# Optimization experiments

Hardware: AMD Instinct MI355X
Metric: run time of the kernel (lower is better)

The kernel has to match this reference:

```python
import jax, jax.numpy as jnp
import numpy as np

HEADS = 16
EMBED = 1024
HEAD_DIM = EMBED // HEADS

def _split_heads(x):
    b, n, _ = x.shape
    return x.reshape(b, n, HEADS, HEAD_DIM).transpose(0, 2, 1, 3)  # b h n d

def _merge_heads(x):
    b, h, n, d = x.shape
    return x.transpose(0, 2, 1, 3).reshape(b, n, h * d)

def _attn(q_in, kv_in, Wq, bq, Wk, bk, Wv, bv, Wo, bo):
    q = _split_heads(q_in @ Wq + bq)
    k = _split_heads(kv_in @ Wk + bk)
    v = _split_heads(kv_in @ Wv + bv)
    e = jnp.einsum('bhqd,bhkd->bhqk', q, k) * (HEAD_DIM ** -0.5)
    a = jax.nn.softmax(e, axis=-1)
    o = jnp.einsum('bhqk,bhkd->bhqd', a, v)
    return _merge_heads(o) @ Wo + bo

def _layernorm(x, g, b, eps=1e-5):
    mu = jnp.mean(x, axis=-1, keepdims=True)
    var = jnp.var(x, axis=-1, keepdims=True)
    return (x - mu) * jax.lax.rsqrt(var + eps) * g + b

def setup_inputs() -> dict:
    key = jax.random.key(0)
    ks = jax.random.split(key, 20)
    s = 0.02
    d = {
        'temp_features': jax.random.normal(ks[0], (2, 2048, EMBED), jnp.float32),
        'spat_features': jax.random.normal(ks[1], (2, 2048, EMBED), jnp.float32),
    }
    names = ['t2s_Wq', 't2s_Wk', 't2s_Wv', 't2s_Wo', 's2t_Wq', 's2t_Wk', 's2t_Wv', 's2t_Wo']
    for i, nm in enumerate(names):
        d[nm] = jax.random.normal(ks[2 + i], (EMBED, EMBED), jnp.float32) * s
        d[nm.replace('W', 'b')] = jnp.zeros((EMBED,), jnp.float32)
    d['ln_g'] = jnp.ones((EMBED,), jnp.float32)
    d['ln_b'] = jnp.zeros((EMBED,), jnp.float32)
    return d

def reference(temp_features, spat_features,
              t2s_Wq, t2s_bq, t2s_Wk, t2s_bk, t2s_Wv, t2s_bv, t2s_Wo, t2s_bo,
              s2t_Wq, s2t_bq, s2t_Wk, s2t_bk, s2t_Wv, s2t_bv, s2t_Wo, s2t_bo,
              ln_g, ln_b):
    # t2s: queries from spat, keys/values from temp; residual = spat
    t2s = _attn(spat_features, temp_features, t2s_Wq, t2s_bq, t2s_Wk, t2s_bk,
                t2s_Wv, t2s_bv, t2s_Wo, t2s_bo)
    t2s_out = _layernorm(spat_features + t2s, ln_g, ln_b)
    # s2t: queries from temp, keys/values from spat; residual = temp
    s2t = _attn(temp_features, spat_features, s2t_Wq, s2t_bq, s2t_Wk, s2t_bk,
                s2t_Wv, s2t_bv, s2t_Wo, s2t_bo)
    s2t_out = _layernorm(temp_features + s2t, ln_g, ln_b)
    return (s2t_out, t2s_out)
```

## Files before the change

kernel.cpp:

```cpp
#include <hip/hip_runtime.h>
#include <stdint.h>

#define SEQ 2048
#define EMB 1024
#define NROWS 4096

typedef __bf16 bf16x8 __attribute__((ext_vector_type(8)));
typedef float f32x4 __attribute__((ext_vector_type(4)));
typedef unsigned short ushort8 __attribute__((ext_vector_type(8)));

__device__ __forceinline__ unsigned short f2bf(float f) {
  unsigned int u = __float_as_uint(f);
  u += 0x7fffu + ((u >> 16) & 1u);
  return (unsigned short)(u >> 16);
}

__device__ __forceinline__ f32x4 mfma16(bf16x8 a, bf16x8 b, f32x4 c) {
  return __builtin_amdgcn_mfma_f32_16x16x32_bf16(a, b, c, 0, 0, 0);
}

__device__ __forceinline__ void async_load16(const void* g, void* l) {
  auto gp = reinterpret_cast<__attribute__((address_space(1))) void*>(
      reinterpret_cast<uintptr_t>(g));
  auto lp = reinterpret_cast<__attribute__((address_space(3))) void*>(
      reinterpret_cast<uintptr_t>(l));
  __builtin_amdgcn_global_load_lds(gp, lp, 16, 0, 0);
}

__global__ __launch_bounds__(256) void cvt2(const float* __restrict__ t,
                                            const float* __restrict__ s,
                                            unsigned short* __restrict__ tb,
                                            unsigned short* __restrict__ sb) {
  const int half = NROWS * EMB / 4 / 4096 * 4096;
  int i = blockIdx.x * 256 + threadIdx.x;
  const float* x; unsigned short* y;
  if (i < NROWS * EMB / 4) { x = (const float*)t; y = tb; }
  else { x = (const float*)s; y = sb; i -= NROWS * EMB / 4; }
  float4 v = ((const float4*)x)[i];
  ushort4 o;
  o.x = f2bf(v.x); o.y = f2bf(v.y); o.z = f2bf(v.z); o.w = f2bf(v.w);
  ((ushort4*)y)[i] = o;
  (void)half;
}

__global__ __launch_bounds__(256) void wtrans8(const float* __restrict__ W0,
                                               const float* __restrict__ W1,
                                               const float* __restrict__ W2,
                                               const float* __restrict__ W3,
                                               const float* __restrict__ W4,
                                               const float* __restrict__ W5,
                                               const float* __restrict__ W6,
                                               const float* __restrict__ W7,
                                               unsigned short* __restrict__ Wt) {
  const float* Ws[8] = {W0, W1, W2, W3, W4, W5, W6, W7};
  const float* W = Ws[blockIdx.z];
  unsigned short* dst = Wt + ((size_t)blockIdx.z << 20);
  __shared__ unsigned short t[64][65];
  const int n0 = blockIdx.x * 64, k0 = blockIdx.y * 64;
#pragma unroll
  for (int i = 0; i < 16; ++i) {
    const int e = i * 256 + threadIdx.x;
    const int kk = e >> 6, nn = e & 63;
    t[kk][nn] = f2bf(W[(size_t)(k0 + kk) * EMB + n0 + nn]);
  }
  __syncthreads();
#pragma unroll
  for (int i = 0; i < 16; ++i) {
    const int e = i * 256 + threadIdx.x;
    const int nn = e >> 6, kk = e & 63;
    dst[(size_t)(n0 + nn) * EMB + k0 + kk] = t[kk][nn];
  }
}

__device__ __forceinline__ void gemm_core128(const unsigned short* __restrict__ A,
                                             const unsigned short* __restrict__ Bt,
                                             int m0, int bt0,
                                             unsigned short* As, unsigned short* Bs,
                                             f32x4 (&acc)[4][4]) {
  const int tid = threadIdx.x;
  const int w = tid >> 6, lane = tid & 63;
  const int quad = lane >> 4, l16 = lane & 15;
  const int wm = w & 1, wn = w >> 1;
  const int srow = lane >> 2, scol = (lane & 3) * 8;
  const unsigned short* Ag = A + (size_t)(m0 + w * 32 + srow) * EMB + scol;
  const unsigned short* Bg = Bt + (size_t)(bt0 + w * 32 + srow) * EMB + scol;
  unsigned short* AsW = As + (w * 32) * 32;
  unsigned short* BsW = Bs + (w * 32) * 32;

  for (int kk = 0; kk < EMB; kk += 32) {
    __syncthreads();
    async_load16(Ag + kk, AsW);
    async_load16(Ag + (size_t)16 * EMB + kk, AsW + 16 * 32);
    async_load16(Bg + kk, BsW);
    async_load16(Bg + (size_t)16 * EMB + kk, BsW + 16 * 32);
    __syncthreads();
    bf16x8 af[4], bfr[4];
#pragma unroll
    for (int im = 0; im < 4; ++im)
      af[im] = *(const bf16x8*)(As + (wm * 64 + im * 16 + l16) * 32 + quad * 8);
#pragma unroll
    for (int in = 0; in < 4; ++in)
      bfr[in] = *(const bf16x8*)(Bs + (wn * 64 + in * 16 + l16) * 32 + quad * 8);
#pragma unroll
    for (int im = 0; im < 4; ++im)
#pragma unroll
      for (int in = 0; in < 4; ++in)
        acc[im][in] = mfma16(af[im], bfr[in], acc[im][in]);
  }
}

__global__ __launch_bounds__(256) void gemm_qkv(const unsigned short* __restrict__ tempb,
                                                const unsigned short* __restrict__ spatb,
                                                const unsigned short* __restrict__ Wt,
                                                const float* __restrict__ bq0,
                                                const float* __restrict__ bk0,
                                                const float* __restrict__ bv0,
                                                const float* __restrict__ bq1,
                                                const float* __restrict__ bk1,
                                                const float* __restrict__ bv1,
                                                unsigned short* __restrict__ Qb,
                                                unsigned short* __restrict__ Kb,
                                                unsigned short* __restrict__ Vtb) {
  __shared__ alignas(16) unsigned short As[128 * 32];
  __shared__ alignas(16) unsigned short Bs[128 * 32];
  const int idx = blockIdx.x >> 3;
  const int dir = idx / 3, kind = idx - dir * 3;
  const int n0 = (blockIdx.x & 7) * 128;
  const unsigned short* A =
      (dir == 0) ? (kind == 0 ? tempb : spatb) : (kind == 0 ? spatb : tempb);
  const float* bias = (dir == 0) ? (kind == 0 ? bq0 : (kind == 1 ? bk0 : bv0))
                                 : (kind == 0 ? bq1 : (kind == 1 ? bk1 : bv1));

  f32x4 acc[4][4] = {};
  gemm_core128(A, Wt + ((size_t)(dir * 4 + kind) << 20), blockIdx.y * 128, n0, As, Bs, acc);

  const int tid = threadIdx.x;
  const int w = tid >> 6, lane = tid & 63;
  const int quad = lane >> 4, l16 = lane & 15;
  const int wm = w & 1, wn = w >> 1;
  const int rowb = blockIdx.y * 128 + wm * 64;
  const size_t dof = (size_t)dir * NROWS * EMB;

  if (kind == 2) {
    unsigned short* Vt = Vtb + dof;
#pragma unroll
    for (int in = 0; in < 4; ++in) {
      const int col = n0 + wn * 64 + in * 16 + l16;
      const int h = col >> 6, d = col & 63;
      const float bvv = bias[col];
#pragma unroll
      for (int im = 0; im < 4; ++im) {
        const int row = rowb + im * 16 + quad * 4;
        const int b = row >> 11, key = row & 2047;
        ushort4 o;
        o.x = f2bf(acc[im][in][0] + bvv);
        o.y = f2bf(acc[im][in][1] + bvv);
        o.z = f2bf(acc[im][in][2] + bvv);
        o.w = f2bf(acc[im][in][3] + bvv);
        *(ushort4*)(Vt + ((size_t)(b * 16 + h) * 64 + d) * SEQ + key) = o;
      }
    }
  } else {
    unsigned short* out = ((kind == 0) ? Qb : Kb) + dof;
    const float scale = (kind == 0) ? 0.18033688011112042f : 1.0f;
#pragma unroll
    for (int in = 0; in < 4; ++in) {
      const int col = n0 + wn * 64 + in * 16 + l16;
      const float bvv = bias[col];
#pragma unroll
      for (int im = 0; im < 4; ++im)
#pragma unroll
        for (int r = 0; r < 4; ++r) {
          const int row = rowb + im * 16 + quad * 4 + r;
          out[(size_t)row * EMB + col] = f2bf((acc[im][in][r] + bvv) * scale);
        }
    }
  }
}

__global__ __launch_bounds__(256) void gemm_o(const unsigned short* __restrict__ Ob,
                                              const unsigned short* __restrict__ Wt,
                                              const float* __restrict__ bo0,
                                              const float* __restrict__ bo1,
                                              const float* __restrict__ temp,
                                              const float* __restrict__ spat,
                                              float* __restrict__ proj) {
  __shared__ alignas(16) unsigned short As[128 * 32];
  __shared__ alignas(16) unsigned short Bs[128 * 32];
  const int dir = blockIdx.x >> 3;
  const int n0 = (blockIdx.x & 7) * 128;
  const size_t dof = (size_t)dir * NROWS * EMB;
  const float* bias = dir ? bo1 : bo0;
  const float* resid = dir ? spat : temp;

  f32x4 acc[4][4] = {};
  gemm_core128(Ob + dof, Wt + ((size_t)(dir * 4 + 3) << 20), blockIdx.y * 128, n0, As, Bs,
               acc);

  const int tid = threadIdx.x;
  const int w = tid >> 6, lane = tid & 63;
  const int quad = lane >> 4, l16 = lane & 15;
  const int wm = w & 1, wn = w >> 1;
  const int rowb = blockIdx.y * 128 + wm * 64;
  float* outf = proj + dof;
#pragma unroll
  for (int in = 0; in < 4; ++in) {
    const int col = n0 + wn * 64 + in * 16 + l16;
    const float bvv = bias[col];
#pragma unroll
    for (int im = 0; im < 4; ++im)
#pragma unroll
      for (int r = 0; r < 4; ++r) {
        const int row = rowb + im * 16 + quad * 4 + r;
        const size_t off = (size_t)row * EMB + col;
        outf[off] = acc[im][in][r] + bvv + resid[off];
      }
  }
}

__global__ __launch_bounds__(256, 4) void flash_attn(const unsigned short* __restrict__ Qall,
                                                     const unsigned short* __restrict__ Kall,
                                                     const unsigned short* __restrict__ Vtall,
                                                     unsigned short* __restrict__ Oall) {
  __shared__ alignas(16) unsigned short Ks[64 * 64];
  __shared__ alignas(16) unsigned short Vs[64 * 64];
  __shared__ alignas(16) unsigned short Ps[4][2048];

  const int tid = threadIdx.x;
  const int w = tid >> 6, lane = tid & 63;
  const int quad = lane >> 4, l16 = lane & 15;
  const int dir = blockIdx.y >> 5, bh = blockIdx.y & 31;
  const int b = bh >> 4, h = bh & 15;
  const size_t dof = (size_t)dir * NROWS * EMB;
  const unsigned short* Q = Qall + dof;
  const unsigned short* K = Kall + dof;
  const unsigned short* Vt = Vtall + dof;
  unsigned short* O = Oall + dof;
  const int q0 = blockIdx.x * 128 + w * 32;

  bf16x8 qf[2][2];
#pragma unroll
  for (int qh = 0; qh < 2; ++qh) {
    const unsigned short* Qrow = Q + (size_t)(b * SEQ + q0 + qh * 16 + l16) * EMB + h * 64;
    qf[qh][0] = *(const bf16x8*)(Qrow + quad * 8);
    qf[qh][1] = *(const bf16x8*)(Qrow + 32 + quad * 8);
  }

  bf16x8 onesf;
#pragma unroll
  for (int i = 0; i < 8; ++i) onesf[i] = (__bf16)1.0f;

  f32x4 oaccT[2][4] = {};
  f32x4 rs[2] = {};
  unsigned short* pw = &Ps[w][0];
  const int swz = (l16 & 7) << 1;
  const int sw8 = l16 & 7;

  const int r8 = lane >> 3, p8 = lane & 7;
  const int kr0 = w * 16 + r8, kr1 = kr0 + 8;
  const unsigned short* Ksrc0 = K + (size_t)(b * SEQ + kr0) * EMB + h * 64 + ((p8 ^ (kr0 & 7)) * 8);
  const unsigned short* Ksrc1 = K + (size_t)(b * SEQ + kr1) * EMB + h * 64 + ((p8 ^ (kr1 & 7)) * 8);
  const unsigned short* Vsrc0 = Vt + ((size_t)bh * 64 + kr0) * SEQ + ((p8 ^ (kr0 & 7)) * 8);
  const unsigned short* Vsrc1 = Vt + ((size_t)bh * 64 + kr1) * SEQ + ((p8 ^ (kr1 & 7)) * 8);
  unsigned short* KsW0 = Ks + (w * 16) * 64;
  unsigned short* KsW1 = Ks + (w * 16 + 8) * 64;
  unsigned short* VsW0 = Vs + (w * 16) * 64;
  unsigned short* VsW1 = Vs + (w * 16 + 8) * 64;

  for (int kt = 0; kt < SEQ; kt += 64) {
    __syncthreads();
    async_load16(Ksrc0 + (size_t)kt * EMB, KsW0);
    async_load16(Ksrc1 + (size_t)kt * EMB, KsW1);
    async_load16(Vsrc0 + kt, VsW0);
    async_load16(Vsrc1 + kt, VsW1);
    __syncthreads();

#pragma unroll
    for (int g = 0; g < 4; ++g) {
      const int key = g * 16 + l16;
      bf16x8 kf0 = *(const bf16x8*)(Ks + key * 64 + ((quad ^ sw8) * 8));
      bf16x8 kf1 = *(const bf16x8*)(Ks + key * 64 + (((4 + quad) ^ sw8) * 8));
      const int kb = 4 * g + quad;
#pragma unroll
      for (int qh = 0; qh < 2; ++qh) {
        f32x4 z = {};
        z = mfma16(kf0, qf[qh][0], z);
        z = mfma16(kf1, qf[qh][1], z);
        uint2 pk;
        pk.x = (__float_as_uint(__builtin_amdgcn_exp2f(z[0])) >> 16) |
               (__float_as_uint(__builtin_amdgcn_exp2f(z[1])) & 0xffff0000u);
        pk.y = (__float_as_uint(__builtin_amdgcn_exp2f(z[2])) >> 16) |
               (__float_as_uint(__builtin_amdgcn_exp2f(z[3])) & 0xffff0000u);
        *(uint2*)(pw + (qh * 16 + l16) * 64 + ((kb ^ swz) << 2)) = pk;
      }
    }
    asm volatile("" ::: "memory");
    bf16x8 pb[2][2];
#pragma unroll
    for (int qh = 0; qh < 2; ++qh) {
      const int qrow = qh * 16 + l16;
      pb[qh][0] = *(const bf16x8*)(pw + qrow * 64 + (((2 * quad) ^ swz) << 2));
      pb[qh][1] = *(const bf16x8*)(pw + qrow * 64 + (((8 + 2 * quad) ^ swz) << 2));
      rs[qh] = mfma16(onesf, pb[qh][1], mfma16(onesf, pb[qh][0], rs[qh]));
    }
    asm volatile("" ::: "memory");
#pragma unroll
    for (int dg = 0; dg < 4; ++dg) {
      const int dd = dg * 16 + l16;
      bf16x8 v0 = *(const bf16x8*)(Vs + dd * 64 + ((quad ^ sw8) * 8));
      bf16x8 v1 = *(const bf16x8*)(Vs + dd * 64 + (((4 + quad) ^ sw8) * 8));
#pragma unroll
      for (int qh = 0; qh < 2; ++qh) {
        oaccT[qh][dg] = mfma16(v0, pb[qh][0], oaccT[qh][dg]);
        oaccT[qh][dg] = mfma16(v1, pb[qh][1], oaccT[qh][dg]);
      }
    }
    asm volatile("" ::: "memory");
  }

#pragma unroll
  for (int qh = 0; qh < 2; ++qh) {
    const float inv = 1.0f / rs[qh][0];
#pragma unroll
    for (int dg = 0; dg < 4; ++dg) {
      uint2 pk;
      pk.x = (unsigned int)f2bf(oaccT[qh][dg][0] * inv) |
             ((unsigned int)f2bf(oaccT[qh][dg][1] * inv) << 16);
      pk.y = (unsigned int)f2bf(oaccT[qh][dg][2] * inv) |
             ((unsigned int)f2bf(oaccT[qh][dg][3] * inv) << 16);
      const int kb = 4 * dg + quad;
      *(uint2*)(pw + l16 * 64 + ((kb ^ swz) << 2)) = pk;
    }
    asm volatile("" ::: "memory");
    const int qq = lane >> 2, cc = lane & 3;
    const int swq = (qq & 7) << 1;
    ushort8 r0 = *(const ushort8*)(pw + qq * 64 + (((4 * cc) ^ swq) << 2));
    ushort8 r1 = *(const ushort8*)(pw + qq * 64 + (((4 * cc + 2) ^ swq) << 2));
    unsigned short* Orow = O + (size_t)(b * SEQ + q0 + qh * 16 + qq) * EMB + h * 64 + cc * 16;
    *(ushort8*)(Orow) = r0;
    *(ushort8*)(Orow + 8) = r1;
    asm volatile("" ::: "memory");
  }
}

__global__ __launch_bounds__(256) void ln_k(const float* __restrict__ X,
                                            const float* __restrict__ g,
                                            const float* __restrict__ bb,
                                            float* __restrict__ out) {
  const int row = blockIdx.x;
  const int tid = threadIdx.x;
  const float4 v = ((const float4*)(X + (size_t)row * EMB))[tid];
  float s = v.x + v.y + v.z + v.w;
  float s2 = v.x * v.x + v.y * v.y + v.z * v.z + v.w * v.w;
#pragma unroll
  for (int o = 32; o > 0; o >>= 1) {
    s += __shfl_down(s, o);
    s2 += __shfl_down(s2, o);
  }
  __shared__ float ws[4], ws2[4];
  if ((tid & 63) == 0) { ws[tid >> 6] = s; ws2[tid >> 6] = s2; }
  __syncthreads();
  const float S = ws[0] + ws[1] + ws[2] + ws[3];
  const float S2 = ws2[0] + ws2[1] + ws2[2] + ws2[3];
  const float mu = S * (1.f / EMB);
  const float inv = rsqrtf(S2 * (1.f / EMB) - mu * mu + 1e-5f);
  const float4 gv = ((const float4*)g)[tid];
  const float4 bv = ((const float4*)bb)[tid];
  float4 o4;
  o4.x = (v.x - mu) * inv * gv.x + bv.x;
  o4.y = (v.y - mu) * inv * gv.y + bv.y;
  o4.z = (v.z - mu) * inv * gv.z + bv.z;
  o4.w = (v.w - mu) * inv * gv.w + bv.w;
  ((float4*)(out + (size_t)row * EMB))[tid] = o4;
}

extern "C" void kernel_launch(void* const* d_in, const int* in_sizes, int n_in,
                              void* d_out, int out_size, void* d_ws, size_t ws_size,
                              hipStream_t stream) {
  const float* temp = (const float*)d_in[0];
  const float* spat = (const float*)d_in[1];
  const float* lng = (const float*)d_in[18];
  const float* lnb = (const float*)d_in[19];
  float* out = (float*)d_out;

  char* base = (char*)d_ws;
  unsigned short* tempb = (unsigned short*)(base + ((size_t)0 << 20));
  unsigned short* spatb = (unsigned short*)(base + ((size_t)8 << 20));
  unsigned short* Wt = (unsigned short*)(base + ((size_t)16 << 20));
  unsigned short* Qb = (unsigned short*)(base + ((size_t)32 << 20));
  unsigned short* Kb = (unsigned short*)(base + ((size_t)48 << 20));
  unsigned short* Vtb = (unsigned short*)(base + ((size_t)64 << 20));
  unsigned short* Ob = (unsigned short*)(base + ((size_t)80 << 20));
  float* proj = (float*)(base + ((size_t)32 << 20));

  cvt2<<<8192, 256, 0, stream>>>(temp, spat, tempb, spatb);
  wtrans8<<<dim3(16, 16, 8), 256, 0, stream>>>(
      (const float*)d_in[10], (const float*)d_in[12], (const float*)d_in[14],
      (const float*)d_in[16], (const float*)d_in[2], (const float*)d_in[4],
      (const float*)d_in[6], (const float*)d_in[8], Wt);
  gemm_qkv<<<dim3(48, 32), 256, 0, stream>>>(
      tempb, spatb, Wt, (const float*)d_in[11], (const float*)d_in[13],
      (const float*)d_in[15], (const float*)d_in[3], (const float*)d_in[5],
      (const float*)d_in[7], Qb, Kb, Vtb);
  flash_attn<<<dim3(16, 64), 256, 0, stream>>>(Qb, Kb, Vtb, Ob);
  gemm_o<<<dim3(16, 32), 256, 0, stream>>>(Ob, Wt, (const float*)d_in[17],
                                           (const float*)d_in[9], temp, spat, proj);
  ln_k<<<2 * NROWS, 256, 0, stream>>>(proj, lng, lnb, out);
}
```

Before: 347.4 us.

## Use 2 waves per attention block with 64 query rows per wave

Flash attention blocks shrink from 4 waves to 2, and each wave now handles 64 query rows instead of 32, so each K/V fragment read from LDS feeds twice as many MFMAs. Each thread issues four async K/V loads per tile instead of two, and the per-wave P buffer doubles in size. The cost is higher register pressure (the accumulators double) and fewer waves per block to hide latency, with the launch bound lowered to 2 blocks per CU.

```diff
diff --git a/kernel.cpp b/kernel.cpp
--- a/kernel.cpp
+++ b/kernel.cpp
@@ -31,7 +31,6 @@
                                             const float* __restrict__ s,
                                             unsigned short* __restrict__ tb,
                                             unsigned short* __restrict__ sb) {
-  const int half = NROWS * EMB / 4 / 4096 * 4096;
   int i = blockIdx.x * 256 + threadIdx.x;
   const float* x; unsigned short* y;
   if (i < NROWS * EMB / 4) { x = (const float*)t; y = tb; }
@@ -40,7 +39,6 @@
   ushort4 o;
   o.x = f2bf(v.x); o.y = f2bf(v.y); o.z = f2bf(v.z); o.w = f2bf(v.w);
   ((ushort4*)y)[i] = o;
-  (void)half;
 }
 
 __global__ __launch_bounds__(256) void wtrans8(const float* __restrict__ W0,
@@ -218,13 +216,13 @@
   }
 }
 
-__global__ __launch_bounds__(256, 4) void flash_attn(const unsigned short* __restrict__ Qall,
+__global__ __launch_bounds__(128, 2) void flash_attn(const unsigned short* __restrict__ Qall,
                                                      const unsigned short* __restrict__ Kall,
                                                      const unsigned short* __restrict__ Vtall,
                                                      unsigned short* __restrict__ Oall) {
   __shared__ alignas(16) unsigned short Ks[64 * 64];
   __shared__ alignas(16) unsigned short Vs[64 * 64];
-  __shared__ alignas(16) unsigned short Ps[4][2048];
+  __shared__ alignas(16) unsigned short Ps[2][4096];
 
   const int tid = threadIdx.x;
   const int w = tid >> 6, lane = tid & 63;
@@ -236,11 +234,11 @@
   const unsigned short* K = Kall + dof;
   const unsigned short* Vt = Vtall + dof;
   unsigned short* O = Oall + dof;
-  const int q0 = blockIdx.x * 128 + w * 32;
-
-  bf16x8 qf[2][2];
-#pragma unroll
-  for (int qh = 0; qh < 2; ++qh) {
+  const int q0 = blockIdx.x * 128 + w * 64;
+
+  bf16x8 qf[4][2];
+#pragma unroll
+  for (int qh = 0; qh < 4; ++qh) {
     const unsigned short* Qrow = Q + (size_t)(b * SEQ + q0 + qh * 16 + l16) * EMB + h * 64;
     qf[qh][0] = *(const bf16x8*)(Qrow + quad * 8);
     qf[qh][1] = *(const bf16x8*)(Qrow + 32 + quad * 8);
@@ -250,29 +248,33 @@
 #pragma unroll
   for (int i = 0; i < 8; ++i) onesf[i] = (__bf16)1.0f;
 
-  f32x4 oaccT[2][4] = {};
-  f32x4 rs[2] = {};
+  f32x4 oaccT[4][4] = {};
+  f32x4 rs[4] = {};
   unsigned short* pw = &Ps[w][0];
   const int swz = (l16 & 7) << 1;
   const int sw8 = l16 & 7;
 
   const int r8 = lane >> 3, p8 = lane & 7;
-  const int kr0 = w * 16 + r8, kr1 = kr0 + 8;
-  const unsigned short* Ksrc0 = K + (size_t)(b * SEQ + kr0) * EMB + h * 64 + ((p8 ^ (kr0 & 7)) * 8);
-  const unsigned short* Ksrc1 = K + (size_t)(b * SEQ + kr1) * EMB + h * 64 + ((p8 ^ (kr1 & 7)) * 8);
-  const unsigned short* Vsrc0 = Vt + ((size_t)bh * 64 + kr0) * SEQ + ((p8 ^ (kr0 & 7)) * 8);
-  const unsigned short* Vsrc1 = Vt + ((size_t)bh * 64 + kr1) * SEQ + ((p8 ^ (kr1 & 7)) * 8);
-  unsigned short* KsW0 = Ks + (w * 16) * 64;
-  unsigned short* KsW1 = Ks + (w * 16 + 8) * 64;
-  unsigned short* VsW0 = Vs + (w * 16) * 64;
-  unsigned short* VsW1 = Vs + (w * 16 + 8) * 64;
+  const int swc = (p8 ^ r8) * 8;
+  const unsigned short* Ksrc[4];
+  const unsigned short* Vsrc[4];
+  unsigned short *KsW[4], *VsW[4];
+#pragma unroll
+  for (int i = 0; i < 4; ++i) {
+    const int row = w * 32 + i * 8 + r8;
+    Ksrc[i] = K + (size_t)(b * SEQ + row) * EMB + h * 64 + swc;
+    Vsrc[i] = Vt + ((size_t)bh * 64 + row) * SEQ + swc;
+    KsW[i] = Ks + (w * 32 + i * 8) * 64;
+    VsW[i] = Vs + (w * 32 + i * 8) * 64;
+  }
 
   for (int kt = 0; kt < SEQ; kt += 64) {
     __syncthreads();
-    async_load16(Ksrc0 + (size_t)kt * EMB, KsW0);
-    async_load16(Ksrc1 + (size_t)kt * EMB, KsW1);
-    async_load16(Vsrc0 + kt, VsW0);
-    async_load16(Vsrc1 + kt, VsW1);
+#pragma unroll
+    for (int i = 0; i < 4; ++i) {
+      async_load16(Ksrc[i] + (size_t)kt * EMB, KsW[i]);
+      async_load16(Vsrc[i] + kt, VsW[i]);
+    }
     __syncthreads();
 
 #pragma unroll
@@ -282,7 +284,7 @@
       bf16x8 kf1 = *(const bf16x8*)(Ks + key * 64 + (((4 + quad) ^ sw8) * 8));
       const int kb = 4 * g + quad;
 #pragma unroll
-      for (int qh = 0; qh < 2; ++qh) {
+      for (int qh = 0; qh < 4; ++qh) {
         f32x4 z = {};
         z = mfma16(kf0, qf[qh][0], z);
         z = mfma16(kf1, qf[qh][1], z);
@@ -295,9 +297,9 @@
       }
     }
     asm volatile("" ::: "memory");
-    bf16x8 pb[2][2];
-#pragma unroll
-    for (int qh = 0; qh < 2; ++qh) {
+    bf16x8 pb[4][2];
+#pragma unroll
+    for (int qh = 0; qh < 4; ++qh) {
       const int qrow = qh * 16 + l16;
       pb[qh][0] = *(const bf16x8*)(pw + qrow * 64 + (((2 * quad) ^ swz) << 2));
       pb[qh][1] = *(const bf16x8*)(pw + qrow * 64 + (((8 + 2 * quad) ^ swz) << 2));
@@ -310,7 +312,7 @@
       bf16x8 v0 = *(const bf16x8*)(Vs + dd * 64 + ((quad ^ sw8) * 8));
       bf16x8 v1 = *(const bf16x8*)(Vs + dd * 64 + (((4 + quad) ^ sw8) * 8));
 #pragma unroll
-      for (int qh = 0; qh < 2; ++qh) {
+      for (int qh = 0; qh < 4; ++qh) {
         oaccT[qh][dg] = mfma16(v0, pb[qh][0], oaccT[qh][dg]);
         oaccT[qh][dg] = mfma16(v1, pb[qh][1], oaccT[qh][dg]);
       }
@@ -319,7 +321,7 @@
   }
 
 #pragma unroll
-  for (int qh = 0; qh < 2; ++qh) {
+  for (int qh = 0; qh < 4; ++qh) {
     const float inv = 1.0f / rs[qh][0];
 #pragma unroll
     for (int dg = 0; dg < 4; ++dg) {
@@ -402,7 +404,7 @@
       tempb, spatb, Wt, (const float*)d_in[11], (const float*)d_in[13],
       (const float*)d_in[15], (const float*)d_in[3], (const float*)d_in[5],
       (const float*)d_in[7], Qb, Kb, Vtb);
-  flash_attn<<<dim3(16, 64), 256, 0, stream>>>(Qb, Kb, Vtb, Ob);
+  flash_attn<<<dim3(16, 64), 128, 0, stream>>>(Qb, Kb, Vtb, Ob);
   gemm_o<<<dim3(16, 32), 256, 0, stream>>>(Ob, Wt, (const float*)d_in[17],
                                            (const float*)d_in[9], temp, spat, proj);
   ln_k<<<2 * NROWS, 256, 0, stream>>>(proj, lng, lnb, out);
```

New measurement: 341.6 us. Within noise of the previous version (-1.7%).

## Double GEMM K-tile to 64 with XOR-swizzled LDS layout

Applied to the files above, without the earlier changes.

The shared GEMM core used by the QKV and output projections now stages 64-wide K slices instead of 32, halving the number of barrier pairs per tile. Global-to-LDS loads are pre-swizzled with an XOR on 16-byte chunks so the MFMA fragment reads from LDS avoid bank conflicts. Launch bounds now request 3 blocks per CU. LDS per block doubles, which may limit occupancy, and loads are still not double-buffered.

```diff
diff --git a/kernel.cpp b/kernel.cpp
--- a/kernel.cpp
+++ b/kernel.cpp
@@ -31,7 +31,6 @@
                                             const float* __restrict__ s,
                                             unsigned short* __restrict__ tb,
                                             unsigned short* __restrict__ sb) {
-  const int half = NROWS * EMB / 4 / 4096 * 4096;
   int i = blockIdx.x * 256 + threadIdx.x;
   const float* x; unsigned short* y;
   if (i < NROWS * EMB / 4) { x = (const float*)t; y = tb; }
@@ -40,7 +39,6 @@
   ushort4 o;
   o.x = f2bf(v.x); o.y = f2bf(v.y); o.z = f2bf(v.z); o.w = f2bf(v.w);
   ((ushort4*)y)[i] = o;
-  (void)half;
 }
 
 __global__ __launch_bounds__(256) void wtrans8(const float* __restrict__ W0,
@@ -72,57 +70,79 @@
   }
 }
 
-__device__ __forceinline__ void gemm_core128(const unsigned short* __restrict__ A,
-                                             const unsigned short* __restrict__ Bt,
-                                             int m0, int bt0,
-                                             unsigned short* As, unsigned short* Bs,
-                                             f32x4 (&acc)[4][4]) {
+__device__ __forceinline__ void gemm_core64(const unsigned short* __restrict__ A,
+                                            const unsigned short* __restrict__ Bt,
+                                            int m0, int bt0,
+                                            unsigned short* As, unsigned short* Bs,
+                                            f32x4 (&acc)[4][4]) {
   const int tid = threadIdx.x;
   const int w = tid >> 6, lane = tid & 63;
   const int quad = lane >> 4, l16 = lane & 15;
   const int wm = w & 1, wn = w >> 1;
-  const int srow = lane >> 2, scol = (lane & 3) * 8;
-  const unsigned short* Ag = A + (size_t)(m0 + w * 32 + srow) * EMB + scol;
-  const unsigned short* Bg = Bt + (size_t)(bt0 + w * 32 + srow) * EMB + scol;
-  unsigned short* AsW = As + (w * 32) * 32;
-  unsigned short* BsW = Bs + (w * 32) * 32;
-
-  for (int kk = 0; kk < EMB; kk += 32) {
+  const int sw8 = l16 & 7;
+
+  const int srow = lane >> 3, p8 = lane & 7;
+  const unsigned short* Ag[4];
+  const unsigned short* Bg[4];
+  unsigned short *AsW[4], *BsW[4];
+#pragma unroll
+  for (int i = 0; i < 4; ++i) {
+    const int r = w * 32 + i * 8 + srow;
+    Ag[i] = A + (size_t)(m0 + r) * EMB + ((p8 ^ (r & 7)) * 8);
+    Bg[i] = Bt + (size_t)(bt0 + r) * EMB + ((p8 ^ (r & 7)) * 8);
+    AsW[i] = As + r * 64 - srow * 64 + srow * 64;
+    BsW[i] = Bs + r * 64 - srow * 64 + srow * 64;
+  }
+  unsigned short* AsB[4];
+  unsigned short* BsB[4];
+#pragma unroll
+  for (int i = 0; i < 4; ++i) {
+    AsB[i] = As + (w * 32 + i * 8) * 64;
+    BsB[i] = Bs + (w * 32 + i * 8) * 64;
+  }
+
+  for (int kk = 0; kk < EMB; kk += 64) {
     __syncthreads();
-    async_load16(Ag + kk, AsW);
-    async_load16(Ag + (size_t)16 * EMB + kk, AsW + 16 * 32);
-    async_load16(Bg + kk, BsW);
-    async_load16(Bg + (size_t)16 * EMB + kk, BsW + 16 * 32);
+#pragma unroll
+    for (int i = 0; i < 4; ++i) {
+      async_load16(Ag[i] + kk, AsB[i]);
+      async_load16(Bg[i] + kk, BsB[i]);
+    }
     __syncthreads();
-    bf16x8 af[4], bfr[4];
-#pragma unroll
-    for (int im = 0; im < 4; ++im)
-      af[im] = *(const bf16x8*)(As + (wm * 64 + im * 16 + l16) * 32 + quad * 8);
-#pragma unroll
-    for (int in = 0; in < 4; ++in)
-      bfr[in] = *(const bf16x8*)(Bs + (wn * 64 + in * 16 + l16) * 32 + quad * 8);
-#pragma unroll
-    for (int im = 0; im < 4; ++im)
+#pragma unroll
+    for (int h = 0; h < 2; ++h) {
+      bf16x8 af[4], bfr[4];
+#pragma unroll
+      for (int im = 0; im < 4; ++im)
+        af[im] = *(const bf16x8*)(As + (wm * 64 + im * 16 + l16) * 64 +
+                                  (((h * 4 + quad) ^ sw8) * 8));
 #pragma unroll
       for (int in = 0; in < 4; ++in)
-        acc[im][in] = mfma16(af[im], bfr[in], acc[im][in]);
-  }
-}
-
-__global__ __launch_bounds__(256) void gemm_qkv(const unsigned short* __restrict__ tempb,
-                                                const unsigned short* __restrict__ spatb,
-                                                const unsigned short* __restrict__ Wt,
-                                                const float* __restrict__ bq0,
-                                                const float* __restrict__ bk0,
-                                                const float* __restrict__ bv0,
-                                                const float* __restrict__ bq1,
-                                                const float* __restrict__ bk1,
-                                                const float* __restrict__ bv1,
-                                                unsigned short* __restrict__ Qb,
-                                                unsigned short* __restrict__ Kb,
-                                                unsigned short* __restrict__ Vtb) {
-  __shared__ alignas(16) unsigned short As[128 * 32];
-  __shared__ alignas(16) unsigned short Bs[128 * 32];
+        bfr[in] = *(const bf16x8*)(Bs + (wn * 64 + in * 16 + l16) * 64 +
+                                   (((h * 4 + quad) ^ sw8) * 8));
+#pragma unroll
+      for (int im = 0; im < 4; ++im)
+#pragma unroll
+        for (int in = 0; in < 4; ++in)
+          acc[im][in] = mfma16(af[im], bfr[in], acc[im][in]);
+    }
+  }
+}
+
+__global__ __launch_bounds__(256, 3) void gemm_qkv(const unsigned short* __restrict__ tempb,
+                                                   const unsigned short* __restrict__ spatb,
+                                                   const unsigned short* __restrict__ Wt,
+                                                   const float* __restrict__ bq0,
+                                                   const float* __restrict__ bk0,
+                                                   const float* __restrict__ bv0,
+                                                   const float* __restrict__ bq1,
+                                                   const float* __restrict__ bk1,
+                                                   const float* __restrict__ bv1,
+                                                   unsigned short* __restrict__ Qb,
+                                                   unsigned short* __restrict__ Kb,
+                                                   unsigned short* __restrict__ Vtb) {
+  __shared__ alignas(16) unsigned short As[128 * 64];
+  __shared__ alignas(16) unsigned short Bs[128 * 64];
   const int idx = blockIdx.x >> 3;
   const int dir = idx / 3, kind = idx - dir * 3;
   const int n0 = (blockIdx.x & 7) * 128;
@@ -132,7 +152,7 @@
                                  : (kind == 0 ? bq1 : (kind == 1 ? bk1 : bv1));
 
   f32x4 acc[4][4] = {};
-  gemm_core128(A, Wt + ((size_t)(dir * 4 + kind) << 20), blockIdx.y * 128, n0, As, Bs, acc);
+  gemm_core64(A, Wt + ((size_t)(dir * 4 + kind) << 20), blockIdx.y * 128, n0, As, Bs, acc);
 
   const int tid = threadIdx.x;
   const int w = tid >> 6, lane = tid & 63;
@@ -178,15 +198,15 @@
   }
 }
 
-__global__ __launch_bounds__(256) void gemm_o(const unsigned short* __restrict__ Ob,
-                                              const unsigned short* __restrict__ Wt,
-                                              const float* __restrict__ bo0,
-                                              const float* __restrict__ bo1,
-                                              const float* __restrict__ temp,
-                                              const float* __restrict__ spat,
-                                              float* __restrict__ proj) {
-  __shared__ alignas(16) unsigned short As[128 * 32];
-  __shared__ alignas(16) unsigned short Bs[128 * 32];
+__global__ __launch_bounds__(256, 3) void gemm_o(const unsigned short* __restrict__ Ob,
+                                                 const unsigned short* __restrict__ Wt,
+                                                 const float* __restrict__ bo0,
+                                                 const float* __restrict__ bo1,
+                                                 const float* __restrict__ temp,
+                                                 const float* __restrict__ spat,
+                                                 float* __restrict__ proj) {
+  __shared__ alignas(16) unsigned short As[128 * 64];
+  __shared__ alignas(16) unsigned short Bs[128 * 64];
   const int dir = blockIdx.x >> 3;
   const int n0 = (blockIdx.x & 7) * 128;
   const size_t dof = (size_t)dir * NROWS * EMB;
@@ -194,8 +214,8 @@
   const float* resid = dir ? spat : temp;
 
   f32x4 acc[4][4] = {};
-  gemm_core128(Ob + dof, Wt + ((size_t)(dir * 4 + 3) << 20), blockIdx.y * 128, n0, As, Bs,
-               acc);
+  gemm_core64(Ob + dof, Wt + ((size_t)(dir * 4 + 3) << 20), blockIdx.y * 128, n0, As, Bs,
+              acc);
 
   const int tid = threadIdx.x;
   const int w = tid >> 6, lane = tid & 63;
```

Measured after the change: 331.5 us. -4.6%, faster.
